# Kernel tuning notes

Hardware: AMD Instinct MI355X
Metric: run time of the kernel (lower is better)

## Reference

```python
import jax, jax.numpy as jnp
import numpy as np

N, F, P, E, HID = 50000, 4, 12, 1_600_000, 64  # nodes, input feats, periods (FH), edges, hidden


def setup_inputs() -> dict:
    key = jax.random.key(0)
    ks = jax.random.split(key, 16)

    def nrm(k, shp, scale=0.1):
        return jax.random.normal(k, shp, jnp.float32) * scale

    inp = {
        "x": jax.random.normal(ks[0], (N, F, P), jnp.float32),
        "edge_index": jax.random.randint(ks[1], (2, E), 0, N),
        "edge_weights": jax.random.uniform(ks[2], (E,), jnp.float32),
        "att": nrm(ks[3], (P,), 1.0),
    }
    i = 4
    for g in ("z", "r", "h"):  # TGCN gate params: GCNConv weight/bias + Linear(2*hid, hid)
        inp[f"Wg_{g}"] = nrm(ks[i], (F, HID))
        inp[f"bg_{g}"] = jnp.zeros((HID,), jnp.float32)
        inp[f"Wl_{g}"] = nrm(jax.random.fold_in(ks[i], 1), (2 * HID, HID))
        inp[f"bl_{g}"] = jnp.zeros((HID,), jnp.float32)
        i += 1
    for j in range(1, 5):
        inp[f"W{j}"] = nrm(ks[i], (HID, HID))
        inp[f"b{j}"] = jnp.zeros((HID,), jnp.float32)
        i += 1
    inp["Wo"] = nrm(ks[i], (HID, P * F))
    inp["bo"] = jnp.zeros((P * F,), jnp.float32)
    return inp


def _gcn_norm(edge_index, ew):
    # GCNConv default: add self loops (weight 1), symmetric D^-1/2 (A+I) D^-1/2 normalization
    src, dst = edge_index[0], edge_index[1]
    loop = jnp.arange(N)
    src_f = jnp.concatenate([src, loop])
    dst_f = jnp.concatenate([dst, loop])
    ew_f = jnp.concatenate([ew, jnp.ones((N,), ew.dtype)])
    deg = jax.ops.segment_sum(ew_f, dst_f, num_segments=N)
    dinv = jnp.where(deg > 0, jax.lax.rsqrt(deg), 0.0)
    norm = dinv[src_f] * ew_f * dinv[dst_f]
    return src_f, dst_f, norm


def _gcn(x, W, b, src, dst, norm):
    xw = x @ W                               # [N, HID] transform before propagate
    msg = xw[src] * norm[:, None]            # gather + scale, [E+N, HID]
    return jax.ops.segment_sum(msg, dst, num_segments=N) + b


def reference(x, edge_index, edge_weights, att,
              Wg_z, bg_z, Wl_z, bl_z,
              Wg_r, bg_r, Wl_r, bl_r,
              Wg_h, bg_h, Wl_h, bl_h,
              W1, b1, W2, b2, W3, b3, W4, b4, Wo, bo):
    src, dst, norm = _gcn_norm(edge_index, edge_weights)

    def tgcn_cell(xt):
        # A3TGCN passes H=None every period -> H starts at zeros each period
        Hz = jnp.zeros((xt.shape[0], HID), xt.dtype)
        z = jax.nn.sigmoid(jnp.concatenate([_gcn(xt, Wg_z, bg_z, src, dst, norm), Hz], -1) @ Wl_z + bl_z)
        r = jax.nn.sigmoid(jnp.concatenate([_gcn(xt, Wg_r, bg_r, src, dst, norm), Hz], -1) @ Wl_r + bl_r)
        htil = jnp.tanh(jnp.concatenate([_gcn(xt, Wg_h, bg_h, src, dst, norm), Hz * r], -1) @ Wl_h + bl_h)
        return z * Hz + (1.0 - z) * htil

    probs = jax.nn.softmax(att)
    h = jnp.zeros((N, HID), x.dtype)
    for p in range(P):  # small fixed period loop keeps peak memory at one period's messages
        h = h + probs[p] * tgcn_cell(x[:, :, p])

    h = jax.nn.relu(h)
    h = h @ W1 + b1
    h = h @ W2 + b2
    h = h @ W3 + b3
    h = h @ W4 + b4
    h = h @ Wo + bo                          # [N, FH*F]
    return h.reshape(-1, F, P)
```

## Files before the change

### kernel.cpp

```cpp
#include <hip/hip_runtime.h>
#include <hip/hip_fp16.h>

#define FP 48
#define HID 64
#define NP 12
#define PL 65
#define NBB 1024
#define CAPB 9216

__device__ __forceinline__ void mm_stage(const float* __restrict__ Alds,
                                         const float* __restrict__ Wg,
                                         float* __restrict__ Clds, int t)
{
    const int rg = (t >> 4) * 4, cg = (t & 15) * 4;
    float acc[4][4] = {};
    for (int k = 0; k < 64; ++k) {
        float a0 = Alds[(rg + 0) * PL + k];
        float a1 = Alds[(rg + 1) * PL + k];
        float a2 = Alds[(rg + 2) * PL + k];
        float a3 = Alds[(rg + 3) * PL + k];
        const float4 bv = *reinterpret_cast<const float4*>(Wg + k * 64 + cg);
        acc[0][0] += a0 * bv.x; acc[0][1] += a0 * bv.y; acc[0][2] += a0 * bv.z; acc[0][3] += a0 * bv.w;
        acc[1][0] += a1 * bv.x; acc[1][1] += a1 * bv.y; acc[1][2] += a1 * bv.z; acc[1][3] += a1 * bv.w;
        acc[2][0] += a2 * bv.x; acc[2][1] += a2 * bv.y; acc[2][2] += a2 * bv.z; acc[2][3] += a2 * bv.w;
        acc[3][0] += a3 * bv.x; acc[3][1] += a3 * bv.y; acc[3][2] += a3 * bv.z; acc[3][3] += a3 * bv.w;
    }
    for (int i = 0; i < 4; ++i)
        for (int j = 0; j < 4; ++j)
            Clds[(rg + i) * PL + cg + j] = acc[i][j];
}

__device__ __forceinline__ void bias_stage(const float* __restrict__ bin,
                                           const float* __restrict__ Wg,
                                           const float* __restrict__ badd,
                                           float* __restrict__ bout, int t)
{
    if (t < 64) {
        float s = badd[t];
        for (int k = 0; k < 64; ++k) s += bin[k] * Wg[k * 64 + t];
        bout[t] = s;
    }
}

__device__ void do_prep(
    const float* __restrict__ att,
    const float* __restrict__ Wg_z, const float* __restrict__ bg_z,
    const float* __restrict__ Wl_z, const float* __restrict__ bl_z,
    const float* __restrict__ Wg_h, const float* __restrict__ bg_h,
    const float* __restrict__ Wl_h, const float* __restrict__ bl_h,
    const float* __restrict__ W1, const float* __restrict__ b1,
    const float* __restrict__ W2, const float* __restrict__ b2,
    const float* __restrict__ W3, const float* __restrict__ b3,
    const float* __restrict__ W4, const float* __restrict__ b4,
    const float* __restrict__ Wo, const float* __restrict__ bo,
    float* __restrict__ probs, float* __restrict__ Mz, float* __restrict__ cz,
    float* __restrict__ Mh, float* __restrict__ ch,
    float* __restrict__ Wc, float* __restrict__ bc, int t)
{
    __shared__ float A[64 * PL];
    __shared__ float B[64 * PL];
    __shared__ float bias[64];
    __shared__ float bias2[64];

    if (t == 0) {
        float m = att[0];
        for (int p = 1; p < NP; ++p) m = fmaxf(m, att[p]);
        float e[NP]; float s = 0.f;
        for (int p = 0; p < NP; ++p) { e[p] = __expf(att[p] - m); s += e[p]; }
        float inv = 1.f / s;
        for (int p = 0; p < NP; ++p) probs[p] = e[p] * inv;
    }

    {
        int f = t >> 6, j = t & 63;
        float az = 0.f, ah = 0.f;
        for (int k = 0; k < HID; ++k) {
            az += Wg_z[f * HID + k] * Wl_z[k * HID + j];
            ah += Wg_h[f * HID + k] * Wl_h[k * HID + j];
        }
        Mz[t] = az; Mh[t] = ah;
    }
    if (t < HID) {
        float az = bl_z[t], ah = bl_h[t];
        for (int k = 0; k < HID; ++k) {
            az += bg_z[k] * Wl_z[k * HID + t];
            ah += bg_h[k] * Wl_h[k * HID + t];
        }
        cz[t] = az; ch[t] = ah;
    }

    for (int idx = t; idx < 4096; idx += 256) {
        int i = idx >> 6, j = idx & 63;
        A[i * PL + j] = W1[idx];
    }
    if (t < 64) bias[t] = b1[t];
    __syncthreads();

    mm_stage(A, W2, B, t);
    bias_stage(bias, W2, b2, bias2, t);
    __syncthreads();
    mm_stage(B, W3, A, t);
    bias_stage(bias2, W3, b3, bias, t);
    __syncthreads();
    mm_stage(A, W4, B, t);
    bias_stage(bias, W4, b4, bias2, t);
    __syncthreads();

    const int rg = (t >> 4) * 4, cg = (t & 15) * 4;
    if (cg < FP) {
        float acc[4][4] = {};
        for (int k = 0; k < 64; ++k) {
            float a0 = B[(rg + 0) * PL + k];
            float a1 = B[(rg + 1) * PL + k];
            float a2 = B[(rg + 2) * PL + k];
            float a3 = B[(rg + 3) * PL + k];
            const float4 bv = *reinterpret_cast<const float4*>(Wo + k * FP + cg);
            acc[0][0] += a0 * bv.x; acc[0][1] += a0 * bv.y; acc[0][2] += a0 * bv.z; acc[0][3] += a0 * bv.w;
            acc[1][0] += a1 * bv.x; acc[1][1] += a1 * bv.y; acc[1][2] += a1 * bv.z; acc[1][3] += a1 * bv.w;
            acc[2][0] += a2 * bv.x; acc[2][1] += a2 * bv.y; acc[2][2] += a2 * bv.z; acc[2][3] += a2 * bv.w;
            acc[3][0] += a3 * bv.x; acc[3][1] += a3 * bv.y; acc[3][2] += a3 * bv.z; acc[3][3] += a3 * bv.w;
        }
        for (int i = 0; i < 4; ++i)
            for (int j = 0; j < 4; ++j)
                Wc[(rg + i) * FP + cg + j] = acc[i][j];
    }
    if (t < FP) {
        float s = bo[t];
        for (int k = 0; k < 64; ++k) s += bias2[k] * Wo[k * FP + t];
        bc[t] = s;
    }
}

__global__ __launch_bounds__(256) void build_kernel(
    const int* __restrict__ src, const int* __restrict__ dst,
    const float* __restrict__ ew,
    unsigned* __restrict__ cursor, int2* __restrict__ binned,
    int E, int CE, int NBUK,
    const float* __restrict__ att,
    const float* __restrict__ Wg_z, const float* __restrict__ bg_z,
    const float* __restrict__ Wl_z, const float* __restrict__ bl_z,
    const float* __restrict__ Wg_h, const float* __restrict__ bg_h,
    const float* __restrict__ Wl_h, const float* __restrict__ bl_h,
    const float* __restrict__ W1, const float* __restrict__ b1,
    const float* __restrict__ W2, const float* __restrict__ b2,
    const float* __restrict__ W3, const float* __restrict__ b3,
    const float* __restrict__ W4, const float* __restrict__ b4,
    const float* __restrict__ Wo, const float* __restrict__ bo,
    float* __restrict__ probs, float* __restrict__ Mz, float* __restrict__ cz,
    float* __restrict__ Mh, float* __restrict__ ch,
    float* __restrict__ Wc, float* __restrict__ bc)
{
    const int t = threadIdx.x;
    if (blockIdx.x == NBB) {
        do_prep(att, Wg_z, bg_z, Wl_z, bl_z, Wg_h, bg_h, Wl_h, bl_h,
                W1, b1, W2, b2, W3, b3, W4, b4, Wo, bo,
                probs, Mz, cz, Mh, ch, Wc, bc, t);
        return;
    }
    __shared__ int cnt[256];
    __shared__ int off[256];
    const int base = blockIdx.x * CE;
    const int endb = min(base + CE, E);
    cnt[t] = 0;
    __syncthreads();
    for (int e = base + t; e < endb; e += 256)
        atomicAdd(&cnt[((unsigned)dst[e]) >> 8], 1);
    __syncthreads();
    if (t < NBUK) {
        const int c = cnt[t];
        off[t] = c ? (int)atomicAdd(&cursor[t], (unsigned)c) : 0;
    }
    __syncthreads();
    for (int e = base + t; e < endb; e += 256) {
        const int d = dst[e];
        const int b = ((unsigned)d) >> 8;
        const int r = atomicAdd(&off[b], 1);
        if (r < CAPB)
            binned[(size_t)b * CAPB + r] =
                make_int2(((d & 255) << 16) | src[e], __float_as_int(ew[e]));
    }
}

__global__ __launch_bounds__(1024) void csr_convert_kernel(
    const int2* __restrict__ binned, const unsigned* __restrict__ cursor,
    unsigned* __restrict__ csr, int2* __restrict__ nodeinfo,
    const float* __restrict__ x,
    unsigned short* __restrict__ xs, int N, int NBUK)
{
    const int t = threadIdx.x;
    const int b = blockIdx.x;
    const int node0 = b << 8;
    const int nend = min(256, N - node0);
    const int ebeg = b * CAPB;
    const int ecnt = min((int)cursor[b], CAPB);
    const int eend = ebeg + ecnt;

    __shared__ int   cnt[256];
    __shared__ float fsum[256];
    __shared__ int   pfx[256];
    __shared__ float sdi[256];

    if (t < 256) { cnt[t] = 0; fsum[t] = 0.f; }
    __syncthreads();

    for (int e = ebeg + t; e < eend; e += 1024) {
        const int2 v = binned[e];
        const int dl = (v.x >> 16) & 255;
        atomicAdd(&cnt[dl], 1);
        atomicAdd(&fsum[dl], __int_as_float(v.y));
    }
    __syncthreads();

    const int myc = (t < 256) ? cnt[t] : 0;
    if (t < 256) pfx[t] = myc;
    __syncthreads();
    for (int off = 1; off < 256; off <<= 1) {
        int tmp = (t >= off && t < 256) ? pfx[t - off] : 0;
        __syncthreads();
        if (t < 256) pfx[t] += tmp;
        __syncthreads();
    }

    if (t < 256) {
        const int excl = pfx[t] - myc;
        const float di = rsqrtf(1.f + fsum[t]);
        sdi[t] = di;
        if (t < nend)
            nodeinfo[node0 + t] = make_int2((myc << 22) | (ebeg + excl), __float_as_int(di));
        cnt[t] = ebeg + excl;
    }
    __syncthreads();

    for (int e = ebeg + t; e < eend; e += 1024) {
        const int2 v = binned[e];
        const int dl = (v.x >> 16) & 255;
        const int pos = atomicAdd(&cnt[dl], 1);
        const float w = __int_as_float(v.y);
        const unsigned hb = (unsigned)__half_as_ushort(__float2half_rn(w));
        csr[pos] = (unsigned)(v.x & 0xffff) | (hb << 16);
    }

    const int gtot = nend * 6;
    for (int g = t; g < gtot; g += 1024) {
        const int nl = g / 6;
        const int q = g - nl * 6;
        const float dsc = sdi[nl];
        const float* xr = x + (size_t)(node0 + nl) * FP + q * 8;
        const float4 v0 = *reinterpret_cast<const float4*>(xr);
        const float4 v1 = *reinterpret_cast<const float4*>(xr + 4);
        unsigned p0 = (unsigned)__half_as_ushort(__float2half_rn(dsc * v0.x)) |
                      ((unsigned)__half_as_ushort(__float2half_rn(dsc * v0.y)) << 16);
        unsigned p1 = (unsigned)__half_as_ushort(__float2half_rn(dsc * v0.z)) |
                      ((unsigned)__half_as_ushort(__float2half_rn(dsc * v0.w)) << 16);
        unsigned p2 = (unsigned)__half_as_ushort(__float2half_rn(dsc * v1.x)) |
                      ((unsigned)__half_as_ushort(__float2half_rn(dsc * v1.y)) << 16);
        unsigned p3 = (unsigned)__half_as_ushort(__float2half_rn(dsc * v1.z)) |
                      ((unsigned)__half_as_ushort(__float2half_rn(dsc * v1.w)) << 16);
        *reinterpret_cast<int4*>(xs + (size_t)(node0 + nl) * FP + q * 8) =
            make_int4((int)p0, (int)p1, (int)p2, (int)p3);
    }
}

#define FMAMIX_LO(acc, xpk, evw) \
    asm("v_fma_mix_f32 %0, %1, %2, %0 op_sel:[0,1,0] op_sel_hi:[1,1,0]" \
        : "+v"(acc) : "v"(xpk), "v"(evw))
#define FMAMIX_HI(acc, xpk, evw) \
    asm("v_fma_mix_f32 %0, %1, %2, %0 op_sel:[1,1,0] op_sel_hi:[1,1,0]" \
        : "+v"(acc) : "v"(xpk), "v"(evw))

__global__ __launch_bounds__(256) void gather_node_kernel(
    const unsigned short* __restrict__ xs, const float* __restrict__ x,
    const int2* __restrict__ nodeinfo,
    const unsigned* __restrict__ csr,
    const float* __restrict__ probs,
    const float* __restrict__ Mz, const float* __restrict__ cz,
    const float* __restrict__ Mh, const float* __restrict__ ch,
    const float* __restrict__ Wc, const float* __restrict__ bc,
    float* __restrict__ out, int N)
{
    __shared__ __align__(16) float sWc[HID * FP];
    __shared__ __align__(16) float sprobs[16];
    __shared__ __align__(16) float yacc[4][384];
    __shared__ __align__(16) float yld[4][FP];
    __shared__ __align__(16) float hld[4][HID];
    for (int i = threadIdx.x; i < HID * FP; i += 256) sWc[i] = Wc[i];
    if (threadIdx.x < NP) sprobs[threadIdx.x] = probs[threadIdx.x];
    __syncthreads();

    const int lane = threadIdx.x & 63;
    const int wib  = threadIdx.x >> 6;
    const int n    = blockIdx.x * 4 + wib;
    if (n >= N) return;

    const int slot = lane >> 3;
    const int q    = lane & 7;
    const bool act = (q < 6);
    const int qc   = act ? q : 5;
    const char* xsb = (const char*)xs;

    const int2 ni = nodeinfo[n];
    const int beg = ni.x & 0x3FFFFF;
    const int end = beg + (int)((unsigned)ni.x >> 22);
    const float di = __int_as_float(ni.y);

    float a0 = 0.f, a1 = 0.f, a2 = 0.f, a3 = 0.f;
    float a4 = 0.f, a5 = 0.f, a6 = 0.f, a7 = 0.f;
    #pragma unroll 2
    for (int e = beg + slot; e < end; e += 8) {
        const unsigned ev = csr[e];
        const unsigned soff = (ev & 0xffffu) * 96u;
        const int4 xv = *reinterpret_cast<const int4*>(xsb + soff + (qc << 4));
        FMAMIX_LO(a0, xv.x, ev); FMAMIX_HI(a1, xv.x, ev);
        FMAMIX_LO(a2, xv.y, ev); FMAMIX_HI(a3, xv.y, ev);
        FMAMIX_LO(a4, xv.z, ev); FMAMIX_HI(a5, xv.z, ev);
        FMAMIX_LO(a6, xv.w, ev); FMAMIX_HI(a7, xv.w, ev);
    }

    if (act) {
        float* dst0 = &yacc[wib][slot * 48 + q * 8];
        *reinterpret_cast<float4*>(dst0)     = make_float4(a0, a1, a2, a3);
        *reinterpret_cast<float4*>(dst0 + 4) = make_float4(a4, a5, a6, a7);
    }

    if (lane < FP) {
        const float* yf = yacc[wib];
        float s = 0.f;
        #pragma unroll
        for (int sl = 0; sl < 8; ++sl) s += yf[sl * 48 + lane];
        float xself = x[(size_t)n * FP + lane];
        float yv = di * s + di * di * xself;
        int f = lane / 12;
        int p = lane - f * 12;
        yld[wib][p * 4 + f] = yv;
    }

    const float mz0 = Mz[lane], mz1 = Mz[64 + lane], mz2 = Mz[128 + lane], mz3 = Mz[192 + lane];
    const float mh0 = Mh[lane], mh1 = Mh[64 + lane], mh2 = Mh[128 + lane], mh3 = Mh[192 + lane];
    const float czv = cz[lane], chv = ch[lane];
    const int   c   = (lane < FP) ? lane : 0;
    const float bcv = bc[c];

    const float* yw = yld[wib];
    float hacc = 0.f;
    #pragma unroll
    for (int p = 0; p < NP; ++p) {
        const float4 v = *reinterpret_cast<const float4*>(yw + p * 4);
        float az = czv + v.x * mz0 + v.y * mz1 + v.z * mz2 + v.w * mz3;
        float ah = chv + v.x * mh0 + v.y * mh1 + v.z * mh2 + v.w * mh3;
        float g  = __builtin_amdgcn_rcpf(1.f + __expf(az));
        float ahc = fminf(fmaxf(ah, -15.f), 15.f);
        float eh = __expf(2.f * ahc);
        float th = 1.f - 2.f * __builtin_amdgcn_rcpf(eh + 1.f);
        hacc += sprobs[p] * g * th;
    }
    hacc = fmaxf(hacc, 0.f);

    hld[wib][lane] = hacc;
    const float* hw = hld[wib];
    float o = bcv;
    #pragma unroll
    for (int i4 = 0; i4 < 16; ++i4) {
        const float4 h4 = *reinterpret_cast<const float4*>(hw + i4 * 4);
        o += h4.x * sWc[(i4 * 4 + 0) * FP + c];
        o += h4.y * sWc[(i4 * 4 + 1) * FP + c];
        o += h4.z * sWc[(i4 * 4 + 2) * FP + c];
        o += h4.w * sWc[(i4 * 4 + 3) * FP + c];
    }
    if (lane < FP) out[(size_t)n * FP + lane] = o;
}

extern "C" void kernel_launch(void* const* d_in, const int* in_sizes, int n_in,
                              void* d_out, int out_size, void* d_ws, size_t ws_size,
                              hipStream_t stream)
{
    const int N = in_sizes[0] / FP;
    const int E = in_sizes[1] / 2;
    const int NBUK = (N + 255) >> 8;
    const int CE = (E + NBB - 1) / NBB;

    const float* x    = (const float*)d_in[0];
    const int*   ei   = (const int*)d_in[1];
    const float* ew   = (const float*)d_in[2];
    const float* att  = (const float*)d_in[3];
    const float* Wg_z = (const float*)d_in[4];
    const float* bg_z = (const float*)d_in[5];
    const float* Wl_z = (const float*)d_in[6];
    const float* bl_z = (const float*)d_in[7];
    const float* Wg_h = (const float*)d_in[12];
    const float* bg_h = (const float*)d_in[13];
    const float* Wl_h = (const float*)d_in[14];
    const float* bl_h = (const float*)d_in[15];
    const float* W1 = (const float*)d_in[16]; const float* b1 = (const float*)d_in[17];
    const float* W2 = (const float*)d_in[18]; const float* b2 = (const float*)d_in[19];
    const float* W3 = (const float*)d_in[20]; const float* b3 = (const float*)d_in[21];
    const float* W4 = (const float*)d_in[22]; const float* b4 = (const float*)d_in[23];
    const float* Wo = (const float*)d_in[24]; const float* bo = (const float*)d_in[25];

    const int* srcp = ei;
    const int* dstp = ei + E;

    int2* binned       = (int2*)d_ws;
    unsigned* csr      = (unsigned*)(binned + (size_t)NBUK * CAPB);
    unsigned short* xs = (unsigned short*)(csr + (size_t)NBUK * CAPB);
    unsigned* cursor   = (unsigned*)(xs + (size_t)N * FP);
    int2* nodeinfo     = (int2*)(cursor + 256);
    float* probs       = (float*)(nodeinfo + N);
    float* Mz          = probs + 16;
    float* cz          = Mz + 256;
    float* Mh          = cz + 64;
    float* ch          = Mh + 256;
    float* Wc          = ch + 64;
    float* bc          = Wc + HID * FP;

    hipMemsetAsync(cursor, 0, (size_t)NBUK * sizeof(unsigned), stream);

    build_kernel<<<NBB + 1, 256, 0, stream>>>(
        srcp, dstp, ew, cursor, binned, E, CE, NBUK,
        att, Wg_z, bg_z, Wl_z, bl_z, Wg_h, bg_h, Wl_h, bl_h,
        W1, b1, W2, b2, W3, b3, W4, b4, Wo, bo,
        probs, Mz, cz, Mh, ch, Wc, bc);

    csr_convert_kernel<<<NBUK, 1024, 0, stream>>>(binned, cursor, csr, nodeinfo,
                                                  x, xs, N, NBUK);

    gather_node_kernel<<<(N + 3) / 4, 256, 0, stream>>>(xs, x, nodeinfo, csr,
                                                        probs, Mz, cz, Mh, ch, Wc, bc,
                                                        (float*)d_out, N);
}
```

Measured before the change: 273.8 us.

## Widen edge buckets to 512 nodes, use 1024-thread build blocks, drop fma_mix asm

Edge binning now groups destinations into 512-node buckets instead of 256, halving the bucket count and roughly doubling per-bucket capacity. The build kernel runs 256 blocks of 1024 threads instead of 1024 blocks of 256, and the prep code is guarded so only the first 256 threads do the matrix stages. The gather loop replaces inline v_fma_mix asm with explicit half-to-float conversions followed by fmaf. The intent is to cut global cursor atomics and block overhead during binning. The trade-off is that the CSR conversion launches only about half as many blocks, which may leave the GPU underused, and the gather loop issues extra conversion instructions.

```diff
diff --git a/kernel.cpp b/kernel.cpp
--- a/kernel.cpp
+++ b/kernel.cpp
@@ -5,8 +5,9 @@
 #define HID 64
 #define NP 12
 #define PL 65
-#define NBB 1024
-#define CAPB 9216
+#define NBB 256
+#define BT 1024
+#define CAPB 17920
 
 __device__ __forceinline__ void mm_stage(const float* __restrict__ Alds,
                                          const float* __restrict__ Wg,
@@ -71,7 +72,7 @@
         for (int p = 0; p < NP; ++p) probs[p] = e[p] * inv;
     }
 
-    {
+    if (t < 256) {
         int f = t >> 6, j = t & 63;
         float az = 0.f, ah = 0.f;
         for (int k = 0; k < HID; ++k) {
@@ -89,49 +90,51 @@
         cz[t] = az; ch[t] = ah;
     }
 
-    for (int idx = t; idx < 4096; idx += 256) {
+    for (int idx = t; idx < 4096; idx += BT) {
         int i = idx >> 6, j = idx & 63;
         A[i * PL + j] = W1[idx];
     }
     if (t < 64) bias[t] = b1[t];
     __syncthreads();
 
-    mm_stage(A, W2, B, t);
+    if (t < 256) mm_stage(A, W2, B, t);
     bias_stage(bias, W2, b2, bias2, t);
     __syncthreads();
-    mm_stage(B, W3, A, t);
+    if (t < 256) mm_stage(B, W3, A, t);
     bias_stage(bias2, W3, b3, bias, t);
     __syncthreads();
-    mm_stage(A, W4, B, t);
+    if (t < 256) mm_stage(A, W4, B, t);
     bias_stage(bias, W4, b4, bias2, t);
     __syncthreads();
 
-    const int rg = (t >> 4) * 4, cg = (t & 15) * 4;
-    if (cg < FP) {
-        float acc[4][4] = {};
-        for (int k = 0; k < 64; ++k) {
-            float a0 = B[(rg + 0) * PL + k];
-            float a1 = B[(rg + 1) * PL + k];
-            float a2 = B[(rg + 2) * PL + k];
-            float a3 = B[(rg + 3) * PL + k];
-            const float4 bv = *reinterpret_cast<const float4*>(Wo + k * FP + cg);
-            acc[0][0] += a0 * bv.x; acc[0][1] += a0 * bv.y; acc[0][2] += a0 * bv.z; acc[0][3] += a0 * bv.w;
-            acc[1][0] += a1 * bv.x; acc[1][1] += a1 * bv.y; acc[1][2] += a1 * bv.z; acc[1][3] += a1 * bv.w;
-            acc[2][0] += a2 * bv.x; acc[2][1] += a2 * bv.y; acc[2][2] += a2 * bv.z; acc[2][3] += a2 * bv.w;
-            acc[3][0] += a3 * bv.x; acc[3][1] += a3 * bv.y; acc[3][2] += a3 * bv.z; acc[3][3] += a3 * bv.w;
+    if (t < 256) {
+        const int rg = (t >> 4) * 4, cg = (t & 15) * 4;
+        if (cg < FP) {
+            float acc[4][4] = {};
+            for (int k = 0; k < 64; ++k) {
+                float a0 = B[(rg + 0) * PL + k];
+                float a1 = B[(rg + 1) * PL + k];
+                float a2 = B[(rg + 2) * PL + k];
+                float a3 = B[(rg + 3) * PL + k];
+                const float4 bv = *reinterpret_cast<const float4*>(Wo + k * FP + cg);
+                acc[0][0] += a0 * bv.x; acc[0][1] += a0 * bv.y; acc[0][2] += a0 * bv.z; acc[0][3] += a0 * bv.w;
+                acc[1][0] += a1 * bv.x; acc[1][1] += a1 * bv.y; acc[1][2] += a1 * bv.z; acc[1][3] += a1 * bv.w;
+                acc[2][0] += a2 * bv.x; acc[2][1] += a2 * bv.y; acc[2][2] += a2 * bv.z; acc[2][3] += a2 * bv.w;
+                acc[3][0] += a3 * bv.x; acc[3][1] += a3 * bv.y; acc[3][2] += a3 * bv.z; acc[3][3] += a3 * bv.w;
+            }
+            for (int i = 0; i < 4; ++i)
+                for (int j = 0; j < 4; ++j)
+                    Wc[(rg + i) * FP + cg + j] = acc[i][j];
         }
-        for (int i = 0; i < 4; ++i)
-            for (int j = 0; j < 4; ++j)
-                Wc[(rg + i) * FP + cg + j] = acc[i][j];
-    }
-    if (t < FP) {
-        float s = bo[t];
-        for (int k = 0; k < 64; ++k) s += bias2[k] * Wo[k * FP + t];
-        bc[t] = s;
-    }
-}
-
-__global__ __launch_bounds__(256) void build_kernel(
+        if (t < FP) {
+            float s = bo[t];
+            for (int k = 0; k < 64; ++k) s += bias2[k] * Wo[k * FP + t];
+            bc[t] = s;
+        }
+    }
+}
+
+__global__ __launch_bounds__(BT) void build_kernel(
     const int* __restrict__ src, const int* __restrict__ dst,
     const float* __restrict__ ew,
     unsigned* __restrict__ cursor, int2* __restrict__ binned,
@@ -157,27 +160,27 @@
                 probs, Mz, cz, Mh, ch, Wc, bc, t);
         return;
     }
-    __shared__ int cnt[256];
-    __shared__ int off[256];
+    __shared__ int cnt[128];
+    __shared__ int off[128];
     const int base = blockIdx.x * CE;
     const int endb = min(base + CE, E);
-    cnt[t] = 0;
-    __syncthreads();
-    for (int e = base + t; e < endb; e += 256)
-        atomicAdd(&cnt[((unsigned)dst[e]) >> 8], 1);
+    if (t < NBUK) cnt[t] = 0;
+    __syncthreads();
+    for (int e = base + t; e < endb; e += BT)
+        atomicAdd(&cnt[((unsigned)dst[e]) >> 9], 1);
     __syncthreads();
     if (t < NBUK) {
         const int c = cnt[t];
         off[t] = c ? (int)atomicAdd(&cursor[t], (unsigned)c) : 0;
     }
     __syncthreads();
-    for (int e = base + t; e < endb; e += 256) {
+    for (int e = base + t; e < endb; e += BT) {
         const int d = dst[e];
-        const int b = ((unsigned)d) >> 8;
+        const int b = ((unsigned)d) >> 9;
         const int r = atomicAdd(&off[b], 1);
         if (r < CAPB)
             binned[(size_t)b * CAPB + r] =
-                make_int2(((d & 255) << 16) | src[e], __float_as_int(ew[e]));
+                make_int2(((d & 511) << 16) | src[e], __float_as_int(ew[e]));
     }
 }
 
@@ -189,39 +192,39 @@
 {
     const int t = threadIdx.x;
     const int b = blockIdx.x;
-    const int node0 = b << 8;
-    const int nend = min(256, N - node0);
+    const int node0 = b << 9;
+    const int nend = min(512, N - node0);
     const int ebeg = b * CAPB;
     const int ecnt = min((int)cursor[b], CAPB);
     const int eend = ebeg + ecnt;
 
-    __shared__ int   cnt[256];
-    __shared__ float fsum[256];
-    __shared__ int   pfx[256];
-    __shared__ float sdi[256];
-
-    if (t < 256) { cnt[t] = 0; fsum[t] = 0.f; }
+    __shared__ int   cnt[512];
+    __shared__ float fsum[512];
+    __shared__ int   pfx[512];
+    __shared__ float sdi[512];
+
+    if (t < 512) { cnt[t] = 0; fsum[t] = 0.f; }
     __syncthreads();
 
     for (int e = ebeg + t; e < eend; e += 1024) {
         const int2 v = binned[e];
-        const int dl = (v.x >> 16) & 255;
+        const int dl = (v.x >> 16) & 511;
         atomicAdd(&cnt[dl], 1);
         atomicAdd(&fsum[dl], __int_as_float(v.y));
     }
     __syncthreads();
 
-    const int myc = (t < 256) ? cnt[t] : 0;
-    if (t < 256) pfx[t] = myc;
-    __syncthreads();
-    for (int off = 1; off < 256; off <<= 1) {
-        int tmp = (t >= off && t < 256) ? pfx[t - off] : 0;
+    const int myc = (t < 512) ? cnt[t] : 0;
+    if (t < 512) pfx[t] = myc;
+    __syncthreads();
+    for (int off = 1; off < 512; off <<= 1) {
+        int tmp = (t >= off && t < 512) ? pfx[t - off] : 0;
         __syncthreads();
-        if (t < 256) pfx[t] += tmp;
+        if (t < 512) pfx[t] += tmp;
         __syncthreads();
     }
 
-    if (t < 256) {
+    if (t < 512) {
         const int excl = pfx[t] - myc;
         const float di = rsqrtf(1.f + fsum[t]);
         sdi[t] = di;
@@ -233,7 +236,7 @@
 
     for (int e = ebeg + t; e < eend; e += 1024) {
         const int2 v = binned[e];
-        const int dl = (v.x >> 16) & 255;
+        const int dl = (v.x >> 16) & 511;
         const int pos = atomicAdd(&cnt[dl], 1);
         const float w = __int_as_float(v.y);
         const unsigned hb = (unsigned)__half_as_ushort(__float2half_rn(w));
@@ -261,13 +264,6 @@
     }
 }
 
-#define FMAMIX_LO(acc, xpk, evw) \
-    asm("v_fma_mix_f32 %0, %1, %2, %0 op_sel:[0,1,0] op_sel_hi:[1,1,0]" \
-        : "+v"(acc) : "v"(xpk), "v"(evw))
-#define FMAMIX_HI(acc, xpk, evw) \
-    asm("v_fma_mix_f32 %0, %1, %2, %0 op_sel:[1,1,0] op_sel_hi:[1,1,0]" \
-        : "+v"(acc) : "v"(xpk), "v"(evw))
-
 __global__ __launch_bounds__(256) void gather_node_kernel(
     const unsigned short* __restrict__ xs, const float* __restrict__ x,
     const int2* __restrict__ nodeinfo,
@@ -308,12 +304,17 @@
     #pragma unroll 2
     for (int e = beg + slot; e < end; e += 8) {
         const unsigned ev = csr[e];
+        const float w = __half2float(__ushort_as_half((unsigned short)(ev >> 16)));
         const unsigned soff = (ev & 0xffffu) * 96u;
         const int4 xv = *reinterpret_cast<const int4*>(xsb + soff + (qc << 4));
-        FMAMIX_LO(a0, xv.x, ev); FMAMIX_HI(a1, xv.x, ev);
-        FMAMIX_LO(a2, xv.y, ev); FMAMIX_HI(a3, xv.y, ev);
-        FMAMIX_LO(a4, xv.z, ev); FMAMIX_HI(a5, xv.z, ev);
-        FMAMIX_LO(a6, xv.w, ev); FMAMIX_HI(a7, xv.w, ev);
+        const float2 f0 = __half22float2(*reinterpret_cast<const __half2*>(&xv.x));
+        const float2 f1 = __half22float2(*reinterpret_cast<const __half2*>(&xv.y));
+        const float2 f2 = __half22float2(*reinterpret_cast<const __half2*>(&xv.z));
+        const float2 f3 = __half22float2(*reinterpret_cast<const __half2*>(&xv.w));
+        a0 = fmaf(w, f0.x, a0); a1 = fmaf(w, f0.y, a1);
+        a2 = fmaf(w, f1.x, a2); a3 = fmaf(w, f1.y, a3);
+        a4 = fmaf(w, f2.x, a4); a5 = fmaf(w, f2.y, a5);
+        a6 = fmaf(w, f3.x, a6); a7 = fmaf(w, f3.y, a7);
     }
 
     if (act) {
@@ -375,7 +376,7 @@
 {
     const int N = in_sizes[0] / FP;
     const int E = in_sizes[1] / 2;
-    const int NBUK = (N + 255) >> 8;
+    const int NBUK = (N + 511) >> 9;
     const int CE = (E + NBB - 1) / NBB;
 
     const float* x    = (const float*)d_in[0];
@@ -403,7 +404,7 @@
     unsigned* csr      = (unsigned*)(binned + (size_t)NBUK * CAPB);
     unsigned short* xs = (unsigned short*)(csr + (size_t)NBUK * CAPB);
     unsigned* cursor   = (unsigned*)(xs + (size_t)N * FP);
-    int2* nodeinfo     = (int2*)(cursor + 256);
+    int2* nodeinfo     = (int2*)(cursor + 128);
     float* probs       = (float*)(nodeinfo + N);
     float* Mz          = probs + 16;
     float* cz          = Mz + 256;
@@ -414,7 +415,7 @@
 
     hipMemsetAsync(cursor, 0, (size_t)NBUK * sizeof(unsigned), stream);
 
-    build_kernel<<<NBB + 1, 256, 0, stream>>>(
+    build_kernel<<<NBB + 1, BT, 0, stream>>>(
         srcp, dstp, ew, cursor, binned, E, CE, NBUK,
         att, Wg_z, bg_z, Wl_z, bl_z, Wg_h, bg_h, Wl_h, bl_h,
         W1, b1, W2, b2, W3, b3, W4, b4, Wo, bo,
```

New measurement: 273.3 us. Within noise of the previous version (-0.2%).
